# Performance work log

Measured on AMD Instinct MI355X. Metric: run time of the kernel, lower is better.

The kernel has to match this reference:

```python
import jax, jax.numpy as jnp
import numpy as np

CHUNK = 512

def setup_inputs() -> dict:
    key = jax.random.key(0)
    kq, kk, kv = jax.random.split(key, 3)
    shape = (1, 16, 8192, 64)  # B, H, N, E
    return {
        "query": jax.random.normal(kq, shape, dtype=jnp.float32),
        "key": jax.random.normal(kk, shape, dtype=jnp.float32),
        "value": jax.random.normal(kv, shape, dtype=jnp.float32),
    }

def reference(query, key, value):
    c = CHUNK
    B, H, N, E = query.shape
    nc = N // c  # number of query chunks (N assumed divisible by c)
    scale = 1.0 / (E ** 0.5)
    neg_inf = jnp.finfo(query.dtype).min

    qc = query.reshape(B, H, nc, c, E)
    kc = key.reshape(B, H, nc, c, E)
    vc = value.reshape(B, H, nc, c, E)

    # ---- chunk 0: window is just keys[0:c], standard causal mask ----
    s0 = jnp.einsum('bhqe,bhse->bhqs', qc[:, :, 0], kc[:, :, 0]) * scale
    mask0 = jnp.triu(jnp.ones((c, c), dtype=bool), k=1)
    a0 = jax.nn.softmax(jnp.where(mask0, neg_inf, s0), axis=-1)  # (B,H,c,c)
    o0 = jnp.einsum('bhqs,bhse->bhqe', a0, vc[:, :, 0])           # (B,H,c,E)

    # ---- chunks 1..nc-1: key window = [previous chunk, current chunk] ----
    kw = jnp.concatenate([kc[:, :, :-1], kc[:, :, 1:]], axis=3)  # (B,H,nc-1,2c,E)
    vw = jnp.concatenate([vc[:, :, :-1], vc[:, :, 1:]], axis=3)
    s = jnp.einsum('bhnqe,bhnse->bhnqs', qc[:, :, 1:], kw) * scale  # (B,H,nc-1,c,2c)
    # faithful to torch.triu(ones(q_len, k_len), diagonal=1): row r keeps cols 0..r
    mask = jnp.triu(jnp.ones((c, 2 * c), dtype=bool), k=1)
    a = jax.nn.softmax(jnp.where(mask, neg_inf, s), axis=-1)        # (B,H,nc-1,c,2c)
    o = jnp.einsum('bhnqs,bhnse->bhnqe', a, vw)                     # (B,H,nc-1,c,E)

    output = jnp.concatenate([o0, o.reshape(B, H, (nc - 1) * c, E)], axis=2)  # (B,H,N,E)
    # weights concatenated along the key axis (torch cat dim=3)
    a_rest = jnp.moveaxis(a, 2, 3).reshape(B, H, c, (nc - 1) * 2 * c)
    weights = jnp.concatenate([a0, a_rest], axis=3)  # (B,H,c, c + (nc-1)*2c)
    return output, weights
```

## Files before the change

### kernel.cpp

```cpp
#include <hip/hip_runtime.h>

typedef __bf16 bf16x8 __attribute__((ext_vector_type(8)));
typedef __bf16 bf16x4 __attribute__((ext_vector_type(4)));
typedef float  f32x4  __attribute__((ext_vector_type(4)));

#define NH    16
#define SEQ   8192
#define EDIM  64
#define CHK   512
#define WCOLS 15872
#define OUT0  8388608

#define MFMA(a, b, c) __builtin_amdgcn_mfma_f32_16x16x32_bf16((a), (b), (c), 0, 0, 0)

__global__ __launch_bounds__(256, 2) void chunked_attn_kernel(
    const float* __restrict__ Qg, const float* __restrict__ Kg,
    const float* __restrict__ Vg, float* __restrict__ out)
{
    __shared__ __align__(16) __bf16 lds_kv[2][8192];
    __shared__ __align__(16) __bf16 lds_p[4][2][640];

    const int tid  = threadIdx.x;
    const int lane = tid & 63;
    const int wv   = __builtin_amdgcn_readfirstlane(tid >> 6);
    const int l16  = lane & 15;
    const int quad = lane >> 4;

    const int bid = blockIdx.x;
    const int g   = bid >> 8;
    const int hn  = bid & 255;
    const int h   = hn >> 4;
    const int n   = hn & 15;
    const int ns  = (n == 0) ? 0 : n - 1;

    const size_t qbase = ((size_t)h * SEQ + (size_t)n  * CHK) * EDIM;
    const size_t kbase = ((size_t)h * SEQ + (size_t)ns * CHK) * EDIM;
    float* __restrict__ W = out + OUT0;
    const size_t wrow0   = (size_t)h * CHK;
    const int    colbase = (n == 0) ? 0 : (CHK + (n - 1) * 2 * CHK);

    const int m0    = g * 64 + wv * 16;
    const int tmax  = g * 4 + wv;
    const int qrow  = m0 + l16;
    const int ntile = (g + 2) >> 1;

    const float SC = 0.125f * 1.44269504088896340736f;

    if (n > 0) {
        float* const zp = W + (wrow0 + (size_t)qrow) * WCOLS + colbase + 512 + quad * 4;
        const f32x4 z = {0.f, 0.f, 0.f, 0.f};
        #pragma unroll
        for (int t = 0; t < 32; ++t)
            __builtin_nontemporal_store(z, (f32x4*)(zp + t * 16));
    }

    bf16x8 aq0, aq1;
    {
        const float* qp = Qg + qbase + (size_t)(m0 + l16) * EDIM + quad * 8;
        float4 a = *(const float4*)(qp);
        float4 b = *(const float4*)(qp + 4);
        aq0[0]=(__bf16)(a.x*SC); aq0[1]=(__bf16)(a.y*SC); aq0[2]=(__bf16)(a.z*SC); aq0[3]=(__bf16)(a.w*SC);
        aq0[4]=(__bf16)(b.x*SC); aq0[5]=(__bf16)(b.y*SC); aq0[6]=(__bf16)(b.z*SC); aq0[7]=(__bf16)(b.w*SC);
        a = *(const float4*)(qp + 32);
        b = *(const float4*)(qp + 36);
        aq1[0]=(__bf16)(a.x*SC); aq1[1]=(__bf16)(a.y*SC); aq1[2]=(__bf16)(a.z*SC); aq1[3]=(__bf16)(a.w*SC);
        aq1[4]=(__bf16)(b.x*SC); aq1[5]=(__bf16)(b.y*SC); aq1[6]=(__bf16)(b.z*SC); aq1[7]=(__bf16)(b.w*SC);
    }

    auto stageK = [&](int kt, int slot) {
        #pragma unroll
        for (int it = 0; it < 4; ++it) {
            const int c = tid + it * 256;
            const int s = c >> 3, sub = c & 7;
            const float* src = Kg + kbase + (size_t)(kt * 128 + s) * EDIM + sub * 8;
            const float4 a = *(const float4*)src;
            const float4 b = *(const float4*)(src + 4);
            bf16x8 t;
            t[0] = (__bf16)a.x; t[1] = (__bf16)a.y; t[2] = (__bf16)a.z; t[3] = (__bf16)a.w;
            t[4] = (__bf16)b.x; t[5] = (__bf16)b.y; t[6] = (__bf16)b.z; t[7] = (__bf16)b.w;
            const int idx = ((s >> 4) * 8 + sub) * 16 + (s & 15);
            ((bf16x8*)lds_kv[slot])[idx] = t;
        }
    };
    auto stageV = [&](int kt, int slot) {
        #pragma unroll
        for (int it = 0; it < 4; ++it) {
            const int c = tid + it * 256;
            const int e = c & 63, sb = c >> 6;
            bf16x8 t;
            #pragma unroll
            for (int j = 0; j < 8; ++j)
                t[j] = (__bf16)Vg[kbase + (size_t)(kt * 128 + sb * 8 + j) * EDIM + e];
            const int idx = (((sb >> 2) * 4 + (e >> 4)) * 4 + (sb & 3)) * 16 + (e & 15);
            ((bf16x8*)lds_kv[slot])[idx] = t;
        }
    };

    f32x4 st[32];
    #pragma unroll
    for (int t = 0; t < 32; ++t) st[t] = (f32x4){0.f, 0.f, 0.f, 0.f};

    stageK(0, 0);
    #pragma unroll
    for (int kt = 0; kt < 4; ++kt) {
        if (kt < ntile) {
            __syncthreads();
            if (kt + 1 < ntile) stageK(kt + 1, (kt + 1) & 1);
            const bf16x8* const kf = (const bf16x8*)lds_kv[kt & 1];
            #pragma unroll
            for (int tt = 0; tt < 8; ++tt) {
                const int t = kt * 8 + tt;
                if (t <= tmax) {
                    const int kb = tt * 128 + quad * 16 + l16;
                    f32x4 acc = {0.f, 0.f, 0.f, 0.f};
                    acc = MFMA(kf[kb],      aq0, acc);
                    acc = MFMA(kf[kb + 64], aq1, acc);
                    if (t == tmax) {
                        const int sb = t * 16 + quad * 4;
                        #pragma unroll
                        for (int r = 0; r < 4; ++r)
                            acc[r] = (sb + r <= qrow) ? acc[r] : -3.0e38f;
                    }
                    st[t] = acc;
                }
            }
        }
    }

    float mr = -3.0e38f;
    #pragma unroll
    for (int t = 0; t < 32; ++t) {
        if (t <= tmax) {
            #pragma unroll
            for (int r = 0; r < 4; ++r) mr = fmaxf(mr, st[t][r]);
        }
    }
    mr = fmaxf(mr, __shfl_xor(mr, 16));
    mr = fmaxf(mr, __shfl_xor(mr, 32));

    float lr = 0.f;
    #pragma unroll
    for (int t = 0; t < 32; ++t) {
        if (t <= tmax) {
            #pragma unroll
            for (int r = 0; r < 4; ++r) {
                const float e = __builtin_amdgcn_exp2f(st[t][r] - mr);
                st[t][r] = e;
                lr += e;
            }
        }
    }
    lr += __shfl_xor(lr, 16);
    lr += __shfl_xor(lr, 32);
    const float ri = __builtin_amdgcn_rcpf(lr);

    #pragma unroll
    for (int t = 0; t < 32; ++t) st[t] = st[t] * ri;

    {
        float* const wp = W + (wrow0 + (size_t)qrow) * WCOLS + colbase + quad * 4;
        #pragma unroll
        for (int t = 0; t < 32; ++t)
            __builtin_nontemporal_store(st[t], (f32x4*)(wp + t * 16));
    }

    __syncthreads();
    stageV(0, 0);

    f32x4 o0 = {0,0,0,0}, o1 = {0,0,0,0}, o2 = {0,0,0,0}, o3 = {0,0,0,0};
    #pragma unroll
    for (int kt = 0; kt < 4; ++kt) {
        if (kt < ntile) {
            __syncthreads();
            if (kt + 1 < ntile) stageV(kt + 1, (kt + 1) & 1);
            const bf16x8* const vf = (const bf16x8*)lds_kv[kt & 1];
            #pragma unroll
            for (int pq = 0; pq < 4; ++pq) {
                const int pr = kt * 4 + pq;
                if (2 * pr <= tmax) {
                    __bf16* const pbuf = lds_p[wv][pq & 1];
                    #pragma unroll
                    for (int tt = 0; tt < 2; ++tt) {
                        const int t = pr * 2 + tt;
                        bf16x4 w;
                        #pragma unroll
                        for (int r = 0; r < 4; ++r) w[r] = (__bf16)st[t][r];
                        *(bf16x4*)(pbuf + l16 * 40 + tt * 16 + quad * 4) = w;
                    }
                    const bf16x8 pa = *(const bf16x8*)(pbuf + l16 * 40 + quad * 8);
                    const int vb = pq * 256 + quad * 16 + l16;
                    o0 = MFMA(pa, vf[vb      ], o0);
                    o1 = MFMA(pa, vf[vb +  64], o1);
                    o2 = MFMA(pa, vf[vb + 128], o2);
                    o3 = MFMA(pa, vf[vb + 192], o3);
                }
            }
        }
    }

    const int rq = m0 + quad * 4;
    const size_t ob = qbase + (size_t)rq * EDIM + l16;
    #pragma unroll
    for (int r = 0; r < 4; ++r) {
        __builtin_nontemporal_store(o0[r], out + ob + (size_t)r * EDIM     );
        __builtin_nontemporal_store(o1[r], out + ob + (size_t)r * EDIM + 16);
        __builtin_nontemporal_store(o2[r], out + ob + (size_t)r * EDIM + 32);
        __builtin_nontemporal_store(o3[r], out + ob + (size_t)r * EDIM + 48);
    }
}

extern "C" void kernel_launch(void* const* d_in, const int* in_sizes, int n_in,
                              void* d_out, int out_size, void* d_ws, size_t ws_size,
                              hipStream_t stream) {
    const float* Q = (const float*)d_in[0];
    const float* K = (const float*)d_in[1];
    const float* V = (const float*)d_in[2];
    float* out = (float*)d_out;
    chunked_attn_kernel<<<dim3(2048), dim3(256), 0, stream>>>(Q, K, V, out);
}
```

Measured before the change: 681.3 us.

## Coalesce attention-weight stores via LDS transpose and split zero-fill into separate kernel

The softmax weights are no longer written straight from MFMA-layout registers, where each lane touches a different row. Each wave now stages its 16x128 tile in a padded shared-memory buffer and re-reads it so 32 lanes write one contiguous 512-byte row segment. Zeroing the masked upper half of each weight window moves out of the attention kernel into a separate fill kernel launched first. This aims for fully coalesced writes to the large weight output, at the cost of about 33 KB more LDS per block, an extra launch, and 16-byte vector accesses at a stride of 129 floats that are not 16-byte aligned.

```diff
diff --git a/kernel.cpp b/kernel.cpp
--- a/kernel.cpp
+++ b/kernel.cpp
@@ -13,12 +13,30 @@
 
 #define MFMA(a, b, c) __builtin_amdgcn_mfma_f32_16x16x32_bf16((a), (b), (c), 0, 0, 0)
 
+__global__ __launch_bounds__(256) void zero_fill_kernel(float* __restrict__ W) {
+    const int gid = blockIdx.x * 256 + threadIdx.x;
+    #pragma unroll
+    for (int it = 0; it < 30; ++it) {
+        const int i     = gid + it * 524288;
+        const int j     = i & 127;
+        const int rowid = i >> 7;
+        const int r     = rowid & 511;
+        const int w     = rowid >> 9;
+        const int h     = w / 15;
+        const int n     = w - h * 15 + 1;
+        float* p = W + (size_t)(h * 512 + r) * WCOLS + (size_t)n * 1024 + j * 4;
+        f32x4 z = {0.f, 0.f, 0.f, 0.f};
+        __builtin_nontemporal_store(z, (f32x4*)p);
+    }
+}
+
 __global__ __launch_bounds__(256, 2) void chunked_attn_kernel(
     const float* __restrict__ Qg, const float* __restrict__ Kg,
     const float* __restrict__ Vg, float* __restrict__ out)
 {
     __shared__ __align__(16) __bf16 lds_kv[2][8192];
     __shared__ __align__(16) __bf16 lds_p[4][2][640];
+    __shared__ __align__(16) float  lds_w[4][16 * 129];
 
     const int tid  = threadIdx.x;
     const int lane = tid & 63;
@@ -45,14 +63,6 @@
     const int ntile = (g + 2) >> 1;
 
     const float SC = 0.125f * 1.44269504088896340736f;
-
-    if (n > 0) {
-        float* const zp = W + (wrow0 + (size_t)qrow) * WCOLS + colbase + 512 + quad * 4;
-        const f32x4 z = {0.f, 0.f, 0.f, 0.f};
-        #pragma unroll
-        for (int t = 0; t < 32; ++t)
-            __builtin_nontemporal_store(z, (f32x4*)(zp + t * 16));
-    }
 
     bf16x8 aq0, aq1;
     {
@@ -157,15 +167,28 @@
     #pragma unroll
     for (int t = 0; t < 32; ++t) st[t] = st[t] * ri;
 
-    {
-        float* const wp = W + (wrow0 + (size_t)qrow) * WCOLS + colbase + quad * 4;
-        #pragma unroll
-        for (int t = 0; t < 32; ++t)
-            __builtin_nontemporal_store(st[t], (f32x4*)(wp + t * 16));
-    }
-
     __syncthreads();
     stageV(0, 0);
+
+    {
+        float* const lw = lds_w[wv];
+        const int rr = lane >> 5;
+        const int cc = (lane & 31) * 4;
+        #pragma unroll
+        for (int ch = 0; ch < 4; ++ch) {
+            #pragma unroll
+            for (int tt = 0; tt < 8; ++tt)
+                *(f32x4*)(lw + l16 * 129 + tt * 16 + quad * 4) = st[ch * 8 + tt];
+            #pragma unroll
+            for (int rp = 0; rp < 8; ++rp) {
+                const int row = rp * 2 + rr;
+                const f32x4 v = *(const f32x4*)(lw + row * 129 + cc);
+                __builtin_nontemporal_store(v,
+                    (f32x4*)(W + (wrow0 + (size_t)(m0 + row)) * WCOLS
+                               + colbase + ch * 128 + cc));
+            }
+        }
+    }
 
     f32x4 o0 = {0,0,0,0}, o1 = {0,0,0,0}, o2 = {0,0,0,0}, o3 = {0,0,0,0};
     #pragma unroll
@@ -216,5 +239,6 @@
     const float* K = (const float*)d_in[1];
     const float* V = (const float*)d_in[2];
     float* out = (float*)d_out;
+    zero_fill_kernel<<<dim3(2048), dim3(256), 0, stream>>>(out + OUT0);
     chunked_attn_kernel<<<dim3(2048), dim3(256), 0, stream>>>(Q, K, V, out);
 }
```

New measurement: 633.5 us. 1.08x faster.
